# Kernel tuning notes

Hardware: AMD Instinct MI355X
Metric: run time of the kernel (lower is better)

The kernel has to match this reference:

```python
import jax, jax.numpy as jnp
import numpy as np
from jax import lax

B, S, P, H = 256, 336, 96, 512


def setup_inputs() -> dict:
    key = jax.random.key(0)
    ks = jax.random.split(key, 18)
    def n(k, shape, s=0.05):
        return jax.random.normal(k, shape, dtype=jnp.float32) * s
    return {
        "x": jax.random.normal(ks[0], (B, S, 7), dtype=jnp.float32),
        "lin_enc_w": n(ks[1], (H, 3)), "lin_enc_b": n(ks[2], (H,)),
        "quat_enc_w": n(ks[3], (H, 4)), "quat_enc_b": n(ks[4], (H,)),
        "lin_wih": n(ks[5], (4 * H, H)), "lin_whh": n(ks[6], (4 * H, H)),
        "lin_bih": n(ks[7], (4 * H,)), "lin_bhh": n(ks[8], (4 * H,)),
        "quat_wih": n(ks[9], (4 * H, H)), "quat_whh": n(ks[10], (4 * H, H)),
        "quat_bih": n(ks[11], (4 * H,)), "quat_bhh": n(ks[12], (4 * H,)),
        "lin_dec_w": n(ks[13], (3, H)), "lin_dec_b": n(ks[14], (3,)),
        "quat_dec_w": n(ks[15], (4, H)), "quat_dec_b": n(ks[16], (4,)),
        "pred_len": P,
    }


def _lstm_cell(carry, xt, Wih, Whh, bih, bhh):
    # PyTorch gate order: i, f, g, o
    h, c = carry
    g = xt @ Wih.T + bih + h @ Whh.T + bhh  # [B, 4H]
    i, f, gg, o = jnp.split(g, 4, axis=-1)
    c = jax.nn.sigmoid(f) * c + jax.nn.sigmoid(i) * jnp.tanh(gg)
    h = jax.nn.sigmoid(o) * jnp.tanh(c)
    return (h, c), h


def _branch(xc, We, be, Wih, Whh, bih, bhh, Wd, bd, pred_len):
    e = xc @ We.T + be  # [B, S, H]
    Bn, _, Hn = e.shape
    cell = lambda carry, xt: _lstm_cell(carry, xt, Wih, Whh, bih, bhh)
    z = jnp.zeros((Bn, Hn), e.dtype)
    (h, _), outs = lax.scan(cell, (z, z), jnp.swapaxes(e, 0, 1))  # outs: [S, B, H]
    # Each prediction step feeds h as input to the LSTM with ZERO initial state
    # (the original code does not pass (h, c) back in).
    def pred_step(h, _):
        (hn, _), _ = cell((jnp.zeros_like(h), jnp.zeros_like(h)), h)
        return hn, hn
    _, preds = lax.scan(pred_step, h, None, length=pred_len)  # [P, B, H]
    seq = jnp.concatenate([outs, preds], axis=0)[1:]  # drop first step -> [S+P-1, B, H]
    return jnp.swapaxes(seq, 0, 1) @ Wd.T + bd


def reference(x, lin_enc_w, lin_enc_b, quat_enc_w, quat_enc_b,
              lin_wih, lin_whh, lin_bih, lin_bhh,
              quat_wih, quat_whh, quat_bih, quat_bhh,
              lin_dec_w, lin_dec_b, quat_dec_w, quat_dec_b, pred_len):
    lx = _branch(x[:, :, :3], lin_enc_w, lin_enc_b, lin_wih, lin_whh,
                 lin_bih, lin_bhh, lin_dec_w, lin_dec_b, pred_len)
    rx = _branch(x[:, :, 3:], quat_enc_w, quat_enc_b, quat_wih, quat_whh,
                 quat_bih, quat_bhh, quat_dec_w, quat_dec_b, pred_len)
    return jnp.concatenate([lx, rx], axis=2)  # [B, S+P-1, 7]
```

## Files before the change

### kernel.cpp

```cpp
#include <hip/hip_runtime.h>

#define BB 256
#define SS 336
#define HH 512
#define NT 431
#define NU 432

typedef __attribute__((ext_vector_type(8))) short bf16x8;
typedef __attribute__((ext_vector_type(16))) float f32x16;
typedef __attribute__((ext_vector_type(4))) int i32x4;


__device__ inline unsigned short f2bf(float f) {
    unsigned int u = __float_as_uint(f);
    unsigned int r = (u + 0x7fffu + ((u >> 16) & 1u)) >> 16;
    return (unsigned short)r;
}
__device__ inline float sigm(float x) { return 1.f / (1.f + __expf(-x)); }
__device__ inline float tanh_(float x) { return 2.f / (1.f + __expf(-2.f * x)) - 1.f; }

__device__ inline i32x4 llc_load_b128(const i32x4* p) {
    i32x4 r;
    asm volatile("global_load_dwordx4 %0, %1, off sc0 sc1" : "=v"(r) : "v"(p));
    return r;
}
__device__ inline void llc_store_b128(i32x4* p, i32x4 v) {
    asm volatile("global_store_dwordx4 %0, %1, off sc0 sc1" :: "v"(p), "v"(v) : "memory");
}
__device__ inline void vm_drain() { asm volatile("s_waitcnt vmcnt(0)" ::: "memory"); }

__global__ void k_wfrag(const float* __restrict__ w0, const float* __restrict__ w1,
                        const float* __restrict__ w2, const float* __restrict__ w3,
                        unsigned short* __restrict__ wfrag) {
    int idx = blockIdx.x * 256 + threadIdx.x;
    int mat = idx >> 17;
    int t = idx & 131071;
    int lane = t & 63;
    int kb = (t >> 6) & 31;
    int csub = (t >> 11) & 1;
    int cg = t >> 12;
    const float* W = mat == 0 ? w0 : (mat == 1 ? w1 : (mat == 2 ? w2 : w3));
    int n_local = csub * 32 + (lane & 31);
    int n = (n_local >> 4) * 512 + cg * 16 + (n_local & 15);
    int k0 = kb * 16 + (lane >> 5) * 8;
    const float* src = W + n * 512 + k0;
    unsigned short us[8];
#pragma unroll
    for (int j = 0; j < 8; ++j) us[j] = f2bf(src[j]);
    i32x4 v;
    v.x = us[0] | (us[1] << 16); v.y = us[2] | (us[3] << 16);
    v.z = us[4] | (us[5] << 16); v.w = us[6] | (us[7] << 16);
    ((i32x4*)wfrag)[idx] = v;
}

__global__ void k_mbias(const float* __restrict__ lin_wih, const float* __restrict__ quat_wih,
                        const float* __restrict__ lin_enc_w, const float* __restrict__ quat_enc_w,
                        const float* __restrict__ lin_enc_b, const float* __restrict__ quat_enc_b,
                        const float* __restrict__ lin_bih, const float* __restrict__ lin_bhh,
                        const float* __restrict__ quat_bih, const float* __restrict__ quat_bhh,
                        float* __restrict__ M, float* __restrict__ bE, float* __restrict__ bP) {
    int gid = blockIdx.x * 256 + threadIdx.x;
    int branch = gid >> 11;
    int n = gid & 2047;
    int nf = 3 + branch;
    const float* Wih = branch ? quat_wih : lin_wih;
    const float* We  = branch ? quat_enc_w : lin_enc_w;
    const float* be  = branch ? quat_enc_b : lin_enc_b;
    const float* bih = branch ? quat_bih : lin_bih;
    const float* bhh = branch ? quat_bhh : lin_bhh;
    float m[4] = {0.f, 0.f, 0.f, 0.f};
    float bs = 0.f;
    for (int j = 0; j < 512; ++j) {
        float w = Wih[n * 512 + j];
#pragma unroll
        for (int kf = 0; kf < 4; ++kf)
            if (kf < nf) m[kf] += w * We[j * nf + kf];
        bs += w * be[j];
    }
    float* Mp = M + (branch * 2048 + n) * 4;
#pragma unroll
    for (int kf = 0; kf < 4; ++kf) Mp[kf] = m[kf];
    bE[branch * 2048 + n] = bs + bih[n] + bhh[n];
    bP[branch * 2048 + n] = bih[n] + bhh[n];
}

__global__ void k_zero(i32x4* __restrict__ p) {
    int idx = blockIdx.x * 256 + threadIdx.x;
    p[idx] = i32x4{0, 0, 0, 0};
}

__global__ void k_initout(float* __restrict__ out,
                          const float* __restrict__ lb, const float* __restrict__ qb) {
    int idx = blockIdx.x * 256 + threadIdx.x;
    if (idx < BB * NT * 7) {
        int d = idx % 7;
        out[idx] = d < 3 ? lb[d] : qb[d - 3];
    }
}

__global__ __launch_bounds__(256, 1) void k_persist(
    const float* __restrict__ x,
    const unsigned short* __restrict__ wfrag,
    const float* __restrict__ M, const float* __restrict__ bE, const float* __restrict__ bP,
    const float* __restrict__ lin_dec_w, const float* __restrict__ quat_dec_w,
    unsigned short* __restrict__ hbuf,
    float* __restrict__ out,
    unsigned int* __restrict__ bar) {
    __shared__ i32x4 lds_a[4096];
    __shared__ float g_lds[64 * 65];
    __shared__ float h_tile[64 * 17];
    __shared__ float mE[256];
    __shared__ float bEs[64];
    __shared__ float bPs[64];
    __shared__ float wds[64];

    const int tid = threadIdx.x;
    const int lane = tid & 63;
    const int wv = tid >> 6;
    const int rsub = wv & 1, csub = wv >> 1;
    const int blk = blockIdx.x;
    const int branch = blk >> 7;
    const int rg = (blk >> 5) & 3;
    const int cg = blk & 31;
    const int group = blk >> 5;
    const int nf = 3 + branch;
    const int row = tid & 63;
    const int jbase = tid >> 6;
    const int b = rg * 64 + row;

    {
        int gate = tid >> 6, jj = (tid >> 2) & 15, kf = tid & 3;
        mE[tid] = M[(size_t)(branch * 2048 + gate * 512 + cg * 16 + jj) * 4 + kf];
    }
    if (tid < 64) {
        int gate = tid >> 4, jj = tid & 15;
        bEs[tid] = bE[branch * 2048 + gate * 512 + cg * 16 + jj];
        bPs[tid] = bP[branch * 2048 + gate * 512 + cg * 16 + jj];
        const float* dw = branch ? quat_dec_w : lin_dec_w;
        wds[tid] = (gate < nf) ? dw[gate * 512 + cg * 16 + jj] : 0.f;
    }

    const i32x4* BpE = (const i32x4*)wfrag + (size_t)(branch * 2) * 131072
                       + ((cg * 2 + csub) * 32) * 64 + lane;
    const i32x4* BpP = BpE + 131072;
    i32x4 bw[32];
#pragma unroll
    for (int kb = 0; kb < 32; ++kb) bw[kb] = BpE[kb * 64];

    float creg[4] = {0.f, 0.f, 0.f, 0.f};
    unsigned int* myslot = bar + (size_t)((group << 5) | cg) * 16;

    __syncthreads();

    for (int u = 0; u < NU; ++u) {
        const int is_enc = (u < SS);

        float xv0 = 0.f, xv1 = 0.f, xv2 = 0.f, xv3 = 0.f;
        if (is_enc) {
            const float* xp = x + ((size_t)b * SS + u) * 7 + branch * 3;
            xv0 = xp[0]; xv1 = xp[1]; xv2 = xp[2];
            if (branch) xv3 = xp[3];
        }
        if (u == SS) {
#pragma unroll
            for (int kb = 0; kb < 32; ++kb) bw[kb] = BpP[kb * 64];
        }

        if (u > 0) {
            if (tid < 64) {
                unsigned int* slot = bar + (size_t)((group << 5) | (lane & 31)) * 16;
                while (!__all((int)(__hip_atomic_load(slot, __ATOMIC_RELAXED,
                                                      __HIP_MEMORY_SCOPE_AGENT)
                                    >= (unsigned int)u)))
                    __builtin_amdgcn_s_sleep(2);
            }
            __syncthreads();
        }

        {
            const i32x4* gsrc = (const i32x4*)hbuf + (size_t)(u & 1) * 32768
                                + (size_t)branch * 16384 + rg * 4096 + tid;
            i32x4 av[16];
#pragma unroll
            for (int i = 0; i < 16; ++i) av[i] = llc_load_b128(gsrc + i * 256);
            vm_drain();
            __builtin_amdgcn_sched_barrier(0);
#pragma unroll
            for (int i = 0; i < 16; ++i) lds_a[i * 256 + tid] = av[i];
        }
        __syncthreads();

        f32x16 acc0 = {};
        f32x16 acc1 = {};
        const i32x4* Afrag = lds_a + rsub * 2048 + lane;
#pragma unroll
        for (int kb = 0; kb < 32; kb += 2) {
            i32x4 a0 = Afrag[kb * 64];
            i32x4 a1 = Afrag[(kb + 1) * 64];
            acc0 = __builtin_amdgcn_mfma_f32_32x32x16_bf16(*(const bf16x8*)&a0, *(const bf16x8*)&bw[kb], acc0, 0, 0, 0);
            acc1 = __builtin_amdgcn_mfma_f32_32x32x16_bf16(*(const bf16x8*)&a1, *(const bf16x8*)&bw[kb + 1], acc1, 0, 0, 0);
        }
        int col_l = csub * 32 + (lane & 31);
        int rbase = rsub * 32 + 4 * (lane >> 5);
#pragma unroll
        for (int r = 0; r < 16; ++r) {
            int row_l = rbase + (r & 3) + 8 * (r >> 2);
            g_lds[row_l * 65 + col_l] = acc0[r] + acc1[r];
        }
        __syncthreads();

#pragma unroll
        for (int p = 0; p < 4; ++p) {
            int jj = jbase * 4 + p;
            float gi = g_lds[row * 65 + jj];
            float gf = g_lds[row * 65 + 16 + jj];
            float gc = g_lds[row * 65 + 32 + jj];
            float go = g_lds[row * 65 + 48 + jj];
            if (is_enc) {
                int j4 = jj * 4;
                gi += bEs[jj]      + xv0 * mE[j4]       + xv1 * mE[j4 + 1]       + xv2 * mE[j4 + 2]       + xv3 * mE[j4 + 3];
                gf += bEs[16 + jj] + xv0 * mE[64 + j4]  + xv1 * mE[64 + j4 + 1]  + xv2 * mE[64 + j4 + 2]  + xv3 * mE[64 + j4 + 3];
                gc += bEs[32 + jj] + xv0 * mE[128 + j4] + xv1 * mE[128 + j4 + 1] + xv2 * mE[128 + j4 + 2] + xv3 * mE[128 + j4 + 3];
                go += bEs[48 + jj] + xv0 * mE[192 + j4] + xv1 * mE[192 + j4 + 1] + xv2 * mE[192 + j4 + 2] + xv3 * mE[192 + j4 + 3];
            } else {
                gi += bPs[jj];
                gf += bPs[16 + jj];
                gc += bPs[32 + jj];
                go += bPs[48 + jj];
            }
            float iv = sigm(gi), fv = sigm(gf), gv = tanh_(gc), ov = sigm(go);
            float cn;
            if (is_enc) {
                cn = fv * creg[p] + iv * gv;
                creg[p] = cn;
            } else {
                cn = iv * gv;
            }
            h_tile[row * 17 + jj] = ov * tanh_(cn);
        }
        __syncthreads();

        if (tid < 128) {
            int chunk = tid >> 6;
            int l = tid & 63;
            int row_l = chunk * 32 + (l & 31);
            int jh = (l >> 5) * 8;
            unsigned short us[8];
#pragma unroll
            for (int j = 0; j < 8; ++j) us[j] = f2bf(h_tile[row_l * 17 + jh + j]);
            i32x4 v;
            v.x = us[0] | (us[1] << 16); v.y = us[2] | (us[3] << 16);
            v.z = us[4] | (us[5] << 16); v.w = us[6] | (us[7] << 16);
            int rb = rg * 2 + chunk;
            llc_store_b128((i32x4*)hbuf + (size_t)((u + 1) & 1) * 32768
                           + (size_t)branch * 16384 + (rb * 32 + cg) * 64 + l, v);
        }
        vm_drain();
        __syncthreads();

        if (tid == 0)
            __hip_atomic_store(myslot, (unsigned int)(u + 1), __ATOMIC_RELAXED,
                               __HIP_MEMORY_SCOPE_AGENT);

        if (u >= 1) {
            if (jbase < nf) {
                float s = 0.f;
#pragma unroll
                for (int j2 = 0; j2 < 16; ++j2) s += h_tile[row * 17 + j2] * wds[jbase * 16 + j2];
                unsafeAtomicAdd(out + ((size_t)b * NT + (u - 1)) * 7 + branch * 3 + jbase, s);
            }
        }
    }
}

extern "C" void kernel_launch(void* const* d_in, const int* in_sizes, int n_in,
                              void* d_out, int out_size, void* d_ws, size_t ws_size,
                              hipStream_t stream) {
    const float* x          = (const float*)d_in[0];
    const float* lin_enc_w  = (const float*)d_in[1];
    const float* lin_enc_b  = (const float*)d_in[2];
    const float* quat_enc_w = (const float*)d_in[3];
    const float* quat_enc_b = (const float*)d_in[4];
    const float* lin_wih    = (const float*)d_in[5];
    const float* lin_whh    = (const float*)d_in[6];
    const float* lin_bih    = (const float*)d_in[7];
    const float* lin_bhh    = (const float*)d_in[8];
    const float* quat_wih   = (const float*)d_in[9];
    const float* quat_whh   = (const float*)d_in[10];
    const float* quat_bih   = (const float*)d_in[11];
    const float* quat_bhh   = (const float*)d_in[12];
    const float* lin_dec_w  = (const float*)d_in[13];
    const float* lin_dec_b  = (const float*)d_in[14];
    const float* quat_dec_w = (const float*)d_in[15];
    const float* quat_dec_b = (const float*)d_in[16];
    float* out = (float*)d_out;
    char* ws = (char*)d_ws;

    unsigned short* wfrag = (unsigned short*)(ws + 0);
    unsigned short* hbuf  = (unsigned short*)(ws + 8388608ull);
    unsigned int*   bar   = (unsigned int*)(ws + 9437184ull);
    float* M    = (float*)(ws + 10485760ull);
    float* bE   = (float*)(ws + 10551296ull);
    float* bP   = (float*)(ws + 10567680ull);

    k_wfrag<<<2048, 256, 0, stream>>>(lin_whh, lin_wih, quat_whh, quat_wih, wfrag);
    k_mbias<<<16, 256, 0, stream>>>(lin_wih, quat_wih, lin_enc_w, quat_enc_w,
                                    lin_enc_b, quat_enc_b, lin_bih, lin_bhh,
                                    quat_bih, quat_bhh, M, bE, bP);
    k_zero<<<260, 256, 0, stream>>>((i32x4*)(ws + 8388608ull));
    k_initout<<<3017, 256, 0, stream>>>(out, lin_dec_b, quat_dec_b);

    k_persist<<<256, 256, 0, stream>>>(x, wfrag, M, bE, bP, lin_dec_w, quat_dec_w,
                                       hbuf, out, bar);
}
```

Before: 3.694 ms.

## Compute decoder output from full h in LDS, drop atomics and init kernel

The decoder projection no longer uses per-block partial sums written with float atomic adds over a bias-initialised output. Instead, wave 0 of each block reads the full previous hidden state already staged in LDS and computes complete dot products for two rows. It then writes the final value with the bias added, which lets the separate output init kernel go away. This adds one extra loop iteration to decode the last step and a 64-element serial dot product per lane on wave 0 every step, which may sit on the critical path.

New measurement: 3.592 ms. 2.8% less time.

```diff
diff --git a/kernel.cpp b/kernel.cpp
--- a/kernel.cpp
+++ b/kernel.cpp
@@ -89,20 +89,12 @@
     p[idx] = i32x4{0, 0, 0, 0};
 }
 
-__global__ void k_initout(float* __restrict__ out,
-                          const float* __restrict__ lb, const float* __restrict__ qb) {
-    int idx = blockIdx.x * 256 + threadIdx.x;
-    if (idx < BB * NT * 7) {
-        int d = idx % 7;
-        out[idx] = d < 3 ? lb[d] : qb[d - 3];
-    }
-}
-
 __global__ __launch_bounds__(256, 1) void k_persist(
     const float* __restrict__ x,
     const unsigned short* __restrict__ wfrag,
     const float* __restrict__ M, const float* __restrict__ bE, const float* __restrict__ bP,
     const float* __restrict__ lin_dec_w, const float* __restrict__ quat_dec_w,
+    const float* __restrict__ lin_dec_b, const float* __restrict__ quat_dec_b,
     unsigned short* __restrict__ hbuf,
     float* __restrict__ out,
     unsigned int* __restrict__ bar) {
@@ -112,7 +104,6 @@
     __shared__ float mE[256];
     __shared__ float bEs[64];
     __shared__ float bPs[64];
-    __shared__ float wds[64];
 
     const int tid = threadIdx.x;
     const int lane = tid & 63;
@@ -136,9 +127,15 @@
         int gate = tid >> 4, jj = tid & 15;
         bEs[tid] = bE[branch * 2048 + gate * 512 + cg * 16 + jj];
         bPs[tid] = bP[branch * 2048 + gate * 512 + cg * 16 + jj];
-        const float* dw = branch ? quat_dec_w : lin_dec_w;
-        wds[tid] = (gate < nf) ? dw[gate * 512 + cg * 16 + jj] : 0.f;
     }
+
+    const int dr   = lane & 1;
+    const int dd   = (lane >> 1) & 3;
+    const int dseg = lane >> 3;
+    const int drow = cg * 2 + dr;
+    const bool dvalid = dd < nf;
+    const float* dwp = (branch ? quat_dec_w : lin_dec_w) + dd * 512;
+    const float dbias = dvalid ? (branch ? quat_dec_b : lin_dec_b)[dd] : 0.f;
 
     const i32x4* BpE = (const i32x4*)wfrag + (size_t)(branch * 2) * 131072
                        + ((cg * 2 + csub) * 32) * 64 + lane;
@@ -152,7 +149,7 @@
 
     __syncthreads();
 
-    for (int u = 0; u < NU; ++u) {
+    for (int u = 0; u <= NU; ++u) {
         const int is_enc = (u < SS);
 
         float xv0 = 0.f, xv1 = 0.f, xv2 = 0.f, xv3 = 0.f;
@@ -189,6 +186,28 @@
             for (int i = 0; i < 16; ++i) lds_a[i * 256 + tid] = av[i];
         }
         __syncthreads();
+
+        if (u == NU) {
+            if (wv == 0) {
+                float s = 0.f;
+                if (dvalid) {
+                    const unsigned short* hp = (const unsigned short*)lds_a;
+                    int rowb = (drow >> 5) * 16384 + (drow & 31) * 8;
+#pragma unroll
+                    for (int jj = 0; jj < 64; ++jj) {
+                        int j = dseg * 64 + jj;
+                        unsigned short hu = hp[rowb + (j >> 4) * 512 + ((j >> 3) & 1) * 256 + (j & 7)];
+                        s += __uint_as_float(((unsigned int)hu) << 16) * dwp[j];
+                    }
+                }
+                s += __shfl_xor(s, 8);
+                s += __shfl_xor(s, 16);
+                s += __shfl_xor(s, 32);
+                if (dseg == 0 && dvalid)
+                    out[((size_t)(rg * 64 + drow) * NT + (u - 2)) * 7 + branch * 3 + dd] = s + dbias;
+            }
+            break;
+        }
 
         f32x16 acc0 = {};
         f32x16 acc1 = {};
@@ -262,13 +281,23 @@
             __hip_atomic_store(myslot, (unsigned int)(u + 1), __ATOMIC_RELAXED,
                                __HIP_MEMORY_SCOPE_AGENT);
 
-        if (u >= 1) {
-            if (jbase < nf) {
-                float s = 0.f;
-#pragma unroll
-                for (int j2 = 0; j2 < 16; ++j2) s += h_tile[row * 17 + j2] * wds[jbase * 16 + j2];
-                unsafeAtomicAdd(out + ((size_t)b * NT + (u - 1)) * 7 + branch * 3 + jbase, s);
-            }
+        if (u >= 2 && wv == 0) {
+            float s = 0.f;
+            if (dvalid) {
+                const unsigned short* hp = (const unsigned short*)lds_a;
+                int rowb = (drow >> 5) * 16384 + (drow & 31) * 8;
+#pragma unroll
+                for (int jj = 0; jj < 64; ++jj) {
+                    int j = dseg * 64 + jj;
+                    unsigned short hu = hp[rowb + (j >> 4) * 512 + ((j >> 3) & 1) * 256 + (j & 7)];
+                    s += __uint_as_float(((unsigned int)hu) << 16) * dwp[j];
+                }
+            }
+            s += __shfl_xor(s, 8);
+            s += __shfl_xor(s, 16);
+            s += __shfl_xor(s, 32);
+            if (dseg == 0 && dvalid)
+                out[((size_t)(rg * 64 + drow) * NT + (u - 2)) * 7 + branch * 3 + dd] = s + dbias;
         }
     }
 }
@@ -308,8 +337,7 @@
                                     lin_enc_b, quat_enc_b, lin_bih, lin_bhh,
                                     quat_bih, quat_bhh, M, bE, bP);
     k_zero<<<260, 256, 0, stream>>>((i32x4*)(ws + 8388608ull));
-    k_initout<<<3017, 256, 0, stream>>>(out, lin_dec_b, quat_dec_b);
 
     k_persist<<<256, 256, 0, stream>>>(x, wfrag, M, bE, bP, lin_dec_w, quat_dec_w,
-                                       hbuf, out, bar);
-}
+                                       lin_dec_b, quat_dec_b, hbuf, out, bar);
+}
```
